# Kernel tuning notes

Measured on AMD Instinct MI355X. Metric: run time of the kernel, lower is better.

Reference implementation:

```python
import jax, jax.numpy as jnp
import numpy as np

N_NODES = 50000
N_EDGES = 1500000
FEAT = 128
CUTOFF = 5.0


def setup_inputs() -> dict:
    key = jax.random.key(0)
    k_x, k_ei, k_el, k_w = jax.random.split(key, 4)
    x = jax.random.normal(k_x, (N_NODES, FEAT), dtype=jnp.float32)
    edge_index = jax.random.randint(k_ei, (2, N_EDGES), 0, N_NODES, dtype=jnp.int64)
    edge_len = jax.random.uniform(k_el, (N_EDGES,), dtype=jnp.float32) * CUTOFF
    # learned params: equivariant mix (dense linear for scalar irreps, no bias),
    # log of distance scale (init sharpness=6.0), and 1->1 filter linear.
    W_mix = jax.random.normal(k_w, (FEAT, FEAT), dtype=jnp.float32) / np.sqrt(FEAT)
    log_scale = jnp.asarray(np.log(6.0), dtype=jnp.float32)
    filter_w = jnp.asarray(0.7, dtype=jnp.float32)
    filter_b = jnp.asarray(0.1, dtype=jnp.float32)
    return {"x": x, "edge_index": edge_index, "edge_len": edge_len,
            "W_mix": W_mix, "log_scale": log_scale,
            "filter_w": filter_w, "filter_b": filter_b}


def reference(x, edge_index, edge_len, W_mix, log_scale, filter_w, filter_b):
    sender = edge_index[0]
    receiver = edge_index[1]
    n_nodes = x.shape[0]

    scale = jnp.exp(log_scale).astype(edge_len.dtype)
    decay = jnp.exp(-jnp.maximum(edge_len / (scale + 1e-6), 0.0) ** 2)  # [E]
    gate = jax.nn.sigmoid(edge_len * filter_w + filter_b)               # [E]
    weights = jnp.nan_to_num(decay * gate, nan=0.0, posinf=0.0, neginf=0.0)

    # gather-scale-scatter: messages [E, F] -> per-node sum
    messages = weights[:, None].astype(x.dtype) * x[sender]
    agg = jax.ops.segment_sum(messages, receiver, num_segments=n_nodes)
    degree = jax.ops.segment_sum(jnp.ones_like(edge_len), receiver,
                                 num_segments=n_nodes)
    agg = agg / jnp.maximum(degree, 1.0)[:, None].astype(x.dtype)

    return x + agg @ W_mix
```

## Files before the change

kernel.cpp:

```cpp
#include <hip/hip_runtime.h>
#include <math.h>

#define FEAT 128
#define BSHIFT 4
#define BNODES 16
#define CAP 1024
#define NBUCK_MAX 4096

__device__ __forceinline__ float edge_weight(float d, float scale, float fw, float fb) {
    float t = fmaxf(d / scale, 0.0f);
    float decay = expf(-t * t);
    float g = 1.0f / (1.0f + expf(-(d * fw + fb)));
    float w = decay * g;
    if (!isfinite(w)) w = 0.0f;
    return w;
}

__device__ __forceinline__ unsigned int bf16_rne(float f) {
    unsigned int b = __float_as_uint(f);
    return (b + 0x7FFFu + ((b >> 16) & 1u)) >> 16;
}

__global__ __launch_bounds__(256) void convert_count_kernel(
    const float4* __restrict__ x4, uint2* __restrict__ xbf, int n4,
    const int* __restrict__ recv, int* __restrict__ sub,
    int E, int nbuck, int epb, int cblocks) {
    __shared__ int cnt[NBUCK_MAX];
    if ((int)blockIdx.x < cblocks) {
        int i = blockIdx.x * 256 + threadIdx.x;
        if (i >= n4) return;
        float4 v = x4[i];
        uint2 o;
        o.x = (bf16_rne(v.y) << 16) | bf16_rne(v.x);
        o.y = (bf16_rne(v.w) << 16) | bf16_rne(v.z);
        xbf[i] = o;
        return;
    }
    int cb = blockIdx.x - cblocks;
    int tid = threadIdx.x;
    for (int i = tid; i < nbuck; i += 256) cnt[i] = 0;
    __syncthreads();
    int base = cb * epb;
    int end = min(base + epb, E);
    for (int e = base + tid; e < end; e += 256)
        atomicAdd(&cnt[recv[e] >> BSHIFT], 1);
    __syncthreads();
    size_t row = (size_t)cb * nbuck;
    for (int i = tid; i < nbuck; i += 256) sub[row + i] = cnt[i];
}

__global__ __launch_bounds__(256) void colscan_kernel(int* __restrict__ sub,
                                                      int* __restrict__ tot,
                                                      int nbuck, int nchunk) {
    __shared__ int vals[256];
    int b = blockIdx.x;
    int tid = threadIdx.x;
    int carry = 0;
    for (int c0 = 0; c0 < nchunk; c0 += 256) {
        int c = c0 + tid;
        int v = (c < nchunk) ? sub[(size_t)c * nbuck + b] : 0;
        vals[tid] = v;
        __syncthreads();
        for (int d = 1; d < 256; d <<= 1) {
            int t = (tid >= d) ? vals[tid - d] : 0;
            __syncthreads();
            vals[tid] += t;
            __syncthreads();
        }
        int excl = vals[tid] - v;
        if (c < nchunk) sub[(size_t)c * nbuck + b] = carry + excl;
        int btot = vals[255];
        __syncthreads();
        carry += btot;
    }
    if (tid == 0) tot[b] = carry;
}

__global__ __launch_bounds__(1024) void scan_kernel(const int* __restrict__ tot,
                                                    int* __restrict__ boff, int M) {
    __shared__ int part[1024];
    int t = threadIdx.x;
    int chunk = (M + 1023) >> 10;
    int lo = t * chunk, hi = min(lo + chunk, M);
    int s = 0;
    for (int i = lo; i < hi; ++i) s += tot[i];
    part[t] = s;
    __syncthreads();
    for (int d = 1; d < 1024; d <<= 1) {
        int v = (t >= d) ? part[t - d] : 0;
        __syncthreads();
        part[t] += v;
        __syncthreads();
    }
    int run = part[t] - s;
    for (int i = lo; i < hi; ++i) {
        boff[i] = run;
        run += tot[i];
    }
    if (hi == M) boff[M] = run;
}

__global__ __launch_bounds__(256) void bucket_scatter_kernel(
    const int* __restrict__ sender, const int* __restrict__ recv,
    const float* __restrict__ edge_len,
    const float* __restrict__ log_scale, const float* __restrict__ filter_w,
    const float* __restrict__ filter_b,
    const int* __restrict__ sub, const int* __restrict__ boff,
    unsigned long long* __restrict__ buf, int E, int nbuck, int epb) {
    __shared__ int cur[NBUCK_MAX];
    int tid = threadIdx.x;
    size_t row = (size_t)blockIdx.x * nbuck;
    for (int i = tid; i < nbuck; i += 256) cur[i] = boff[i] + sub[row + i];
    __syncthreads();
    int base = blockIdx.x * epb;
    int end = min(base + epb, E);
    float scale = expf(log_scale[0]) + 1e-6f;
    float fw = filter_w[0], fb = filter_b[0];
    for (int e = base + tid; e < end; e += 256) {
        int r = recv[e];
        int s = sender[e];
        float w = edge_weight(edge_len[e], scale, fw, fb);
        int pos = atomicAdd(&cur[r >> BSHIFT], 1);
        unsigned long long rec = ((unsigned long long)__float_as_uint(w) << 32)
                               | (unsigned int)(s & 0xFFFF)
                               | ((unsigned int)(r & (BNODES - 1)) << 16);
        buf[pos] = rec;
    }
}

__device__ __forceinline__ void accum8(float acc[8], uint4 u, float w) {
    acc[0] = fmaf(w, __uint_as_float(u.x << 16), acc[0]);
    acc[1] = fmaf(w, __uint_as_float(u.x & 0xFFFF0000u), acc[1]);
    acc[2] = fmaf(w, __uint_as_float(u.y << 16), acc[2]);
    acc[3] = fmaf(w, __uint_as_float(u.y & 0xFFFF0000u), acc[3]);
    acc[4] = fmaf(w, __uint_as_float(u.z << 16), acc[4]);
    acc[5] = fmaf(w, __uint_as_float(u.z & 0xFFFF0000u), acc[5]);
    acc[6] = fmaf(w, __uint_as_float(u.w << 16), acc[6]);
    acc[7] = fmaf(w, __uint_as_float(u.w & 0xFFFF0000u), acc[7]);
}

__global__ __launch_bounds__(256) void bucket_sort_aggregate_kernel(
    const uint4* __restrict__ xbf4, const unsigned long long* __restrict__ buf,
    const int* __restrict__ boff, uint4* __restrict__ agg_bf4,
    int* __restrict__ deg, int N) {
    __shared__ unsigned long long recS[CAP];
    __shared__ int cnt16[BNODES];
    __shared__ int segoff[BNODES + 1];

    int b = blockIdx.x;
    int n0 = b << BSHIFT;
    int nEnd = min(n0 + BNODES, N);
    int lo = boff[b], hi = boff[b + 1];
    int tid = threadIdx.x;
    int lane = tid & 15;
    int grp = tid >> 4;

    float acc[8] = {0.f,0.f,0.f,0.f,0.f,0.f,0.f,0.f};
    int dcnt = 0;

    for (int pos = lo; pos < hi; pos += CAP) {
        int cnt = min(CAP, hi - pos);
        if (tid < BNODES) cnt16[tid] = 0;
        __syncthreads();

        unsigned long long rec[CAP / 256];
        int rnk[CAP / 256];
        int locl[CAP / 256];
#pragma unroll
        for (int k = 0; k < CAP / 256; ++k) {
            int i = k * 256 + tid;
            if (i < cnt) {
                unsigned long long r = buf[pos + i];
                int l = ((unsigned int)r >> 16) & (BNODES - 1);
                rec[k] = r;
                locl[k] = l;
                rnk[k] = atomicAdd(&cnt16[l], 1);
            }
        }
        __syncthreads();
        if (tid == 0) {
            int run = 0;
#pragma unroll
            for (int l = 0; l < BNODES; ++l) { segoff[l] = run; run += cnt16[l]; }
            segoff[BNODES] = run;
        }
        __syncthreads();
#pragma unroll
        for (int k = 0; k < CAP / 256; ++k) {
            int i = k * 256 + tid;
            if (i < cnt) recS[segoff[locl[k]] + rnk[k]] = rec[k];
        }
        __syncthreads();

        {
            int s0 = segoff[grp], s1 = segoff[grp + 1];
            dcnt += s1 - s0;
            int i = s0;
            for (; i + 4 <= s1; i += 4) {
                unsigned long long r0 = recS[i];
                unsigned long long r1 = recS[i + 1];
                unsigned long long r2 = recS[i + 2];
                unsigned long long r3 = recS[i + 3];
                float w0 = __uint_as_float((unsigned int)(r0 >> 32));
                float w1 = __uint_as_float((unsigned int)(r1 >> 32));
                float w2 = __uint_as_float((unsigned int)(r2 >> 32));
                float w3 = __uint_as_float((unsigned int)(r3 >> 32));
                int s0i = (unsigned int)r0 & 0xFFFF;
                int s1i = (unsigned int)r1 & 0xFFFF;
                int s2i = (unsigned int)r2 & 0xFFFF;
                int s3i = (unsigned int)r3 & 0xFFFF;
                uint4 u0 = xbf4[(size_t)s0i * 16 + lane];
                uint4 u1 = xbf4[(size_t)s1i * 16 + lane];
                uint4 u2 = xbf4[(size_t)s2i * 16 + lane];
                uint4 u3 = xbf4[(size_t)s3i * 16 + lane];
                accum8(acc, u0, w0);
                accum8(acc, u1, w1);
                accum8(acc, u2, w2);
                accum8(acc, u3, w3);
            }
            for (; i < s1; ++i) {
                unsigned long long ra = recS[i];
                float wa = __uint_as_float((unsigned int)(ra >> 32));
                int sa = (unsigned int)ra & 0xFFFF;
                uint4 ua = xbf4[(size_t)sa * 16 + lane];
                accum8(acc, ua, wa);
            }
        }
        __syncthreads();
    }

    {
        int n = n0 + grp;
        if (n < nEnd) {
            uint4 o;
            o.x = (bf16_rne(acc[1]) << 16) | bf16_rne(acc[0]);
            o.y = (bf16_rne(acc[3]) << 16) | bf16_rne(acc[2]);
            o.z = (bf16_rne(acc[5]) << 16) | bf16_rne(acc[4]);
            o.w = (bf16_rne(acc[7]) << 16) | bf16_rne(acc[6]);
            agg_bf4[(size_t)n * 16 + lane] = o;
            if (lane == 0) deg[n] = dcnt;
        }
    }
}

__global__ __launch_bounds__(256) void finalize_kernel(
    const float* __restrict__ x, const uint4* __restrict__ agg_bf4,
    const int* __restrict__ deg, const float* __restrict__ Wm,
    float* __restrict__ out, int N) {
    __shared__ float aggS[64 * 128];
    __shared__ float Ws[128 * 64];
    const int n0 = blockIdx.x * 64;

    for (int i = threadIdx.x; i < 64 * 16; i += 256) {
        int r = i >> 4;
        int q = i & 15;
        int n = n0 + r;
        uint4 u = make_uint4(0u, 0u, 0u, 0u);
        if (n < N) u = agg_bf4[(size_t)n * 16 + q];
        float4 f0, f1;
        f0.x = __uint_as_float(u.x << 16);
        f0.y = __uint_as_float(u.x & 0xFFFF0000u);
        f0.z = __uint_as_float(u.y << 16);
        f0.w = __uint_as_float(u.y & 0xFFFF0000u);
        f1.x = __uint_as_float(u.z << 16);
        f1.y = __uint_as_float(u.z & 0xFFFF0000u);
        f1.z = __uint_as_float(u.w << 16);
        f1.w = __uint_as_float(u.w & 0xFFFF0000u);
        int m = (r >> 2) & 7;
        ((float4*)aggS)[r * 32 + ((2 * q) ^ m)] = f0;
        ((float4*)aggS)[r * 32 + ((2 * q + 1) ^ m)] = f1;
    }

    const int tc = threadIdx.x & 15;
    const int tr = threadIdx.x >> 4;

    float invd[4];
#pragma unroll
    for (int i = 0; i < 4; ++i) {
        int n = n0 + 4 * tr + i;
        float degf = 1.0f;
        if (n < N) degf = fmaxf((float)deg[n], 1.0f);
        invd[i] = 1.0f / degf;
    }

    for (int h = 0; h < 2; ++h) {
        for (int i = threadIdx.x; i < 128 * 16; i += 256) {
            int k = i >> 4;
            int j4 = i & 15;
            ((float4*)Ws)[k * 16 + j4] = ((const float4*)Wm)[k * 32 + h * 16 + j4];
        }
        __syncthreads();

        float acc[4][4];
#pragma unroll
        for (int i = 0; i < 4; ++i)
#pragma unroll
            for (int c = 0; c < 4; ++c) acc[i][c] = 0.f;

#pragma unroll 4
        for (int k0 = 0; k0 < 128; k0 += 4) {
            float4 ar4[4];
            const int chunk = (k0 >> 2) ^ (tr & 7);
#pragma unroll
            for (int i = 0; i < 4; ++i) {
                int r = 4 * tr + i;
                ar4[i] = ((const float4*)aggS)[r * 32 + chunk];
            }
            float4 wv4[4];
#pragma unroll
            for (int kk = 0; kk < 4; ++kk)
                wv4[kk] = *(const float4*)&Ws[(k0 + kk) * 64 + tc * 4];

            float wvv[4][4];
#pragma unroll
            for (int kk = 0; kk < 4; ++kk) {
                wvv[kk][0] = wv4[kk].x; wvv[kk][1] = wv4[kk].y;
                wvv[kk][2] = wv4[kk].z; wvv[kk][3] = wv4[kk].w;
            }
#pragma unroll
            for (int i = 0; i < 4; ++i) {
                float av[4] = {ar4[i].x, ar4[i].y, ar4[i].z, ar4[i].w};
#pragma unroll
                for (int kk = 0; kk < 4; ++kk)
#pragma unroll
                    for (int c = 0; c < 4; ++c)
                        acc[i][c] = fmaf(av[kk], wvv[kk][c], acc[i][c]);
            }
        }

#pragma unroll
        for (int i = 0; i < 4; ++i) {
            int n = n0 + 4 * tr + i;
            if (n < N) {
                size_t base = (size_t)n * FEAT + h * 64 + tc * 4;
                float4 xv = *(const float4*)&x[base];
                float4 o;
                o.x = xv.x + invd[i] * acc[i][0];
                o.y = xv.y + invd[i] * acc[i][1];
                o.z = xv.z + invd[i] * acc[i][2];
                o.w = xv.w + invd[i] * acc[i][3];
                *(float4*)&out[base] = o;
            }
        }
        __syncthreads();
    }
}

__global__ __launch_bounds__(256) void scatter_fallback(
    const float4* __restrict__ x4, const int* __restrict__ sender,
    const int* __restrict__ receiver, const float* __restrict__ edge_len,
    const float* __restrict__ log_scale, const float* __restrict__ filter_w,
    const float* __restrict__ filter_b, float* __restrict__ agg,
    float* __restrict__ deg, int E) {
    int gid = blockIdx.x * 256 + threadIdx.x;
    int e = gid >> 5;
    if (e >= E) return;
    int lane = gid & 31;
    int s = sender[e];
    int r = receiver[e];
    float scale = expf(log_scale[0]) + 1e-6f;
    float w = edge_weight(edge_len[e], scale, filter_w[0], filter_b[0]);
    float4 xv = x4[s * (FEAT / 4) + lane];
    float* dst = agg + (size_t)r * FEAT + lane * 4;
    unsafeAtomicAdd(dst + 0, w * xv.x);
    unsafeAtomicAdd(dst + 1, w * xv.y);
    unsafeAtomicAdd(dst + 2, w * xv.z);
    unsafeAtomicAdd(dst + 3, w * xv.w);
    if (lane == 0) unsafeAtomicAdd(&deg[r], 1.0f);
}

__global__ __launch_bounds__(256) void finalize_fallback(
    const float* __restrict__ x, const float* __restrict__ agg,
    const float* __restrict__ deg, const float* __restrict__ Wm,
    float* __restrict__ out, int N) {
    __shared__ float Wsf[FEAT * FEAT];
    for (int i = threadIdx.x * 4; i < FEAT * FEAT; i += 256 * 4)
        *(float4*)&Wsf[i] = *(const float4*)&Wm[i];
    __syncthreads();
    int half = threadIdx.x >> 7;
    int j = threadIdx.x & (FEAT - 1);
    for (int n0 = blockIdx.x * 2; n0 < N; n0 += gridDim.x * 2) {
        int n = n0 + half;
        if (n < N) {
            const float* arow = agg + (size_t)n * FEAT;
            float acc = 0.0f;
#pragma unroll 16
            for (int k = 0; k < FEAT; ++k) acc = fmaf(arow[k], Wsf[k * FEAT + j], acc);
            float invd = 1.0f / fmaxf(deg[n], 1.0f);
            size_t idx = (size_t)n * FEAT + j;
            out[idx] = x[idx] + invd * acc;
        }
    }
}

extern "C" void kernel_launch(void* const* d_in, const int* in_sizes, int n_in,
                              void* d_out, int out_size, void* d_ws, size_t ws_size,
                              hipStream_t stream) {
    const float* x         = (const float*)d_in[0];
    const int*   ei        = (const int*)d_in[1];
    const float* edge_len  = (const float*)d_in[2];
    const float* W_mix     = (const float*)d_in[3];
    const float* log_scale = (const float*)d_in[4];
    const float* filter_w  = (const float*)d_in[5];
    const float* filter_b  = (const float*)d_in[6];
    float* out = (float*)d_out;

    const int N = in_sizes[0] / FEAT;
    const int E = in_sizes[1] / 2;
    const int* sender   = ei;
    const int* receiver = ei + E;
    const int nbuck = (N + BNODES - 1) >> BSHIFT;

    size_t xbf_bytes  = (size_t)N * FEAT * 2;
    size_t aggb_bytes = (size_t)N * FEAT * 2;
    size_t buf_bytes  = (size_t)E * 8;
    size_t tot_bytes  = (((size_t)nbuck * 4) + 63) & ~(size_t)63;
    size_t boff_bytes = (((size_t)(nbuck + 1) * 4) + 63) & ~(size_t)63;
    size_t deg_bytes  = (((size_t)N * 4) + 63) & ~(size_t)63;
    size_t fixed = xbf_bytes + aggb_bytes + buf_bytes + tot_bytes + boff_bytes +
                   deg_bytes;

    int epb = 0, nchunk = 0;
    size_t sub_bytes = 0;
    const int epb_opts[3] = {4096, 8192, 16384};
    for (int oi = 0; oi < 3; ++oi) {
        int cand = epb_opts[oi];
        int nc = (E + cand - 1) / cand;
        size_t sb = (((size_t)nc * nbuck * 4) + 63) & ~(size_t)63;
        if (fixed + sb <= ws_size) { epb = cand; nchunk = nc; sub_bytes = sb; break; }
    }

    if (epb != 0 && N <= 65536) {
        char* p = (char*)d_ws;
        uint2* xbf    = (uint2*)p;                        p += xbf_bytes;
        uint4* agg_bf = (uint4*)p;                        p += aggb_bytes;
        unsigned long long* buf = (unsigned long long*)p; p += buf_bytes;
        int* sub  = (int*)p;                              p += sub_bytes;
        int* tot  = (int*)p;                              p += tot_bytes;
        int* boff = (int*)p;                              p += boff_bytes;
        int* deg  = (int*)p;

        int cblocks = (N * (FEAT / 4) + 255) / 256;
        convert_count_kernel<<<cblocks + nchunk, 256, 0, stream>>>(
            (const float4*)x, xbf, N * (FEAT / 4),
            receiver, sub, E, nbuck, epb, cblocks);
        colscan_kernel<<<nbuck, 256, 0, stream>>>(sub, tot, nbuck, nchunk);
        scan_kernel<<<1, 1024, 0, stream>>>(tot, boff, nbuck);
        bucket_scatter_kernel<<<nchunk, 256, 0, stream>>>(
            sender, receiver, edge_len, log_scale, filter_w, filter_b,
            sub, boff, buf, E, nbuck, epb);
        bucket_sort_aggregate_kernel<<<nbuck, 256, 0, stream>>>(
            (const uint4*)xbf, buf, boff, agg_bf, deg, N);
        int fblocks = (N + 63) / 64;
        finalize_kernel<<<fblocks, 256, 0, stream>>>(x, (const uint4*)agg_bf, deg,
                                                     W_mix, out, N);
    } else {
        float* agg = (float*)d_ws;
        float* degf = agg + (size_t)N * FEAT;
        hipMemsetAsync(agg, 0, ((size_t)N * FEAT + N) * sizeof(float), stream);
        int sblocks = (E * 32 + 255) / 256;
        scatter_fallback<<<sblocks, 256, 0, stream>>>(
            (const float4*)x, sender, receiver, edge_len,
            log_scale, filter_w, filter_b, agg, degf, E);
        finalize_fallback<<<512, 256, 0, stream>>>(x, agg, degf, W_mix, out, N);
    }
}
```

Measured before the change: 238.6 us.

## Replace bucketed two-level sort with per-node CSR via global atomics

Switches from the 16-node bucket sort (per-chunk shared histograms, column scan, and an in-block local sort) to a direct per-receiver CSR: global atomic degree counts, a single scan over nodes, atomic per-node scatter, and an aggregate kernel that reads each node's contiguous edge list with 8-deep prefetch. This removes the colscan kernel, the large sub-count matrix and the shared-memory re-sort in aggregation. The cost is contended global atomics over 50k counters in both the count and scatter passes, a single-block scan over 50k entries, and an extra memset.

```diff
diff --git a/kernel.cpp b/kernel.cpp
--- a/kernel.cpp
+++ b/kernel.cpp
@@ -4,8 +4,6 @@
 #define FEAT 128
 #define BSHIFT 4
 #define BNODES 16
-#define CAP 1024
-#define NBUCK_MAX 4096
 
 __device__ __forceinline__ float edge_weight(float d, float scale, float fw, float fb) {
     float t = fmaxf(d / scale, 0.0f);
@@ -23,9 +21,7 @@
 
 __global__ __launch_bounds__(256) void convert_count_kernel(
     const float4* __restrict__ x4, uint2* __restrict__ xbf, int n4,
-    const int* __restrict__ recv, int* __restrict__ sub,
-    int E, int nbuck, int epb, int cblocks) {
-    __shared__ int cnt[NBUCK_MAX];
+    const int* __restrict__ recv, int* __restrict__ deg, int E, int cblocks) {
     if ((int)blockIdx.x < cblocks) {
         int i = blockIdx.x * 256 + threadIdx.x;
         if (i >= n4) return;
@@ -36,54 +32,21 @@
         xbf[i] = o;
         return;
     }
-    int cb = blockIdx.x - cblocks;
-    int tid = threadIdx.x;
-    for (int i = tid; i < nbuck; i += 256) cnt[i] = 0;
-    __syncthreads();
-    int base = cb * epb;
-    int end = min(base + epb, E);
-    for (int e = base + tid; e < end; e += 256)
-        atomicAdd(&cnt[recv[e] >> BSHIFT], 1);
-    __syncthreads();
-    size_t row = (size_t)cb * nbuck;
-    for (int i = tid; i < nbuck; i += 256) sub[row + i] = cnt[i];
-}
-
-__global__ __launch_bounds__(256) void colscan_kernel(int* __restrict__ sub,
-                                                      int* __restrict__ tot,
-                                                      int nbuck, int nchunk) {
-    __shared__ int vals[256];
-    int b = blockIdx.x;
-    int tid = threadIdx.x;
-    int carry = 0;
-    for (int c0 = 0; c0 < nchunk; c0 += 256) {
-        int c = c0 + tid;
-        int v = (c < nchunk) ? sub[(size_t)c * nbuck + b] : 0;
-        vals[tid] = v;
-        __syncthreads();
-        for (int d = 1; d < 256; d <<= 1) {
-            int t = (tid >= d) ? vals[tid - d] : 0;
-            __syncthreads();
-            vals[tid] += t;
-            __syncthreads();
-        }
-        int excl = vals[tid] - v;
-        if (c < nchunk) sub[(size_t)c * nbuck + b] = carry + excl;
-        int btot = vals[255];
-        __syncthreads();
-        carry += btot;
-    }
-    if (tid == 0) tot[b] = carry;
-}
-
-__global__ __launch_bounds__(1024) void scan_kernel(const int* __restrict__ tot,
-                                                    int* __restrict__ boff, int M) {
+    int nb = gridDim.x - cblocks;
+    int gid = ((int)blockIdx.x - cblocks) * 256 + threadIdx.x;
+    for (int e = gid; e < E; e += nb * 256)
+        atomicAdd(&deg[recv[e]], 1);
+}
+
+__global__ __launch_bounds__(1024) void scan_kernel(const int* __restrict__ deg,
+                                                    int* __restrict__ noff,
+                                                    int* __restrict__ ncur, int M) {
     __shared__ int part[1024];
     int t = threadIdx.x;
     int chunk = (M + 1023) >> 10;
-    int lo = t * chunk, hi = min(lo + chunk, M);
+    int lo = min(t * chunk, M), hi = min(lo + chunk, M);
     int s = 0;
-    for (int i = lo; i < hi; ++i) s += tot[i];
+    for (int i = lo; i < hi; ++i) s += deg[i];
     part[t] = s;
     __syncthreads();
     for (int d = 1; d < 1024; d <<= 1) {
@@ -94,37 +57,29 @@
     }
     int run = part[t] - s;
     for (int i = lo; i < hi; ++i) {
-        boff[i] = run;
-        run += tot[i];
-    }
-    if (hi == M) boff[M] = run;
-}
-
-__global__ __launch_bounds__(256) void bucket_scatter_kernel(
+        noff[i] = run;
+        ncur[i] = run;
+        run += deg[i];
+    }
+    if (hi == M) noff[M] = run;
+}
+
+__global__ __launch_bounds__(256) void scatter_kernel(
     const int* __restrict__ sender, const int* __restrict__ recv,
     const float* __restrict__ edge_len,
     const float* __restrict__ log_scale, const float* __restrict__ filter_w,
     const float* __restrict__ filter_b,
-    const int* __restrict__ sub, const int* __restrict__ boff,
-    unsigned long long* __restrict__ buf, int E, int nbuck, int epb) {
-    __shared__ int cur[NBUCK_MAX];
-    int tid = threadIdx.x;
-    size_t row = (size_t)blockIdx.x * nbuck;
-    for (int i = tid; i < nbuck; i += 256) cur[i] = boff[i] + sub[row + i];
-    __syncthreads();
-    int base = blockIdx.x * epb;
-    int end = min(base + epb, E);
+    int* __restrict__ ncur, unsigned long long* __restrict__ buf, int E) {
     float scale = expf(log_scale[0]) + 1e-6f;
     float fw = filter_w[0], fb = filter_b[0];
-    for (int e = base + tid; e < end; e += 256) {
+    int stride = gridDim.x * 256;
+    for (int e = blockIdx.x * 256 + threadIdx.x; e < E; e += stride) {
         int r = recv[e];
         int s = sender[e];
         float w = edge_weight(edge_len[e], scale, fw, fb);
-        int pos = atomicAdd(&cur[r >> BSHIFT], 1);
-        unsigned long long rec = ((unsigned long long)__float_as_uint(w) << 32)
-                               | (unsigned int)(s & 0xFFFF)
-                               | ((unsigned int)(r & (BNODES - 1)) << 16);
-        buf[pos] = rec;
+        int pos = atomicAdd(&ncur[r], 1);
+        buf[pos] = ((unsigned long long)__float_as_uint(w) << 32)
+                 | (unsigned int)s;
     }
 }
 
@@ -139,108 +94,52 @@
     acc[7] = fmaf(w, __uint_as_float(u.w & 0xFFFF0000u), acc[7]);
 }
 
-__global__ __launch_bounds__(256) void bucket_sort_aggregate_kernel(
+__global__ __launch_bounds__(256) void aggregate_kernel(
     const uint4* __restrict__ xbf4, const unsigned long long* __restrict__ buf,
-    const int* __restrict__ boff, uint4* __restrict__ agg_bf4,
-    int* __restrict__ deg, int N) {
-    __shared__ unsigned long long recS[CAP];
-    __shared__ int cnt16[BNODES];
-    __shared__ int segoff[BNODES + 1];
-
-    int b = blockIdx.x;
-    int n0 = b << BSHIFT;
-    int nEnd = min(n0 + BNODES, N);
-    int lo = boff[b], hi = boff[b + 1];
-    int tid = threadIdx.x;
-    int lane = tid & 15;
-    int grp = tid >> 4;
-
-    float acc[8] = {0.f,0.f,0.f,0.f,0.f,0.f,0.f,0.f};
-    int dcnt = 0;
-
-    for (int pos = lo; pos < hi; pos += CAP) {
-        int cnt = min(CAP, hi - pos);
-        if (tid < BNODES) cnt16[tid] = 0;
-        __syncthreads();
-
-        unsigned long long rec[CAP / 256];
-        int rnk[CAP / 256];
-        int locl[CAP / 256];
-#pragma unroll
-        for (int k = 0; k < CAP / 256; ++k) {
-            int i = k * 256 + tid;
-            if (i < cnt) {
-                unsigned long long r = buf[pos + i];
-                int l = ((unsigned int)r >> 16) & (BNODES - 1);
-                rec[k] = r;
-                locl[k] = l;
-                rnk[k] = atomicAdd(&cnt16[l], 1);
-            }
-        }
-        __syncthreads();
-        if (tid == 0) {
-            int run = 0;
-#pragma unroll
-            for (int l = 0; l < BNODES; ++l) { segoff[l] = run; run += cnt16[l]; }
-            segoff[BNODES] = run;
-        }
-        __syncthreads();
-#pragma unroll
-        for (int k = 0; k < CAP / 256; ++k) {
-            int i = k * 256 + tid;
-            if (i < cnt) recS[segoff[locl[k]] + rnk[k]] = rec[k];
-        }
-        __syncthreads();
-
-        {
-            int s0 = segoff[grp], s1 = segoff[grp + 1];
-            dcnt += s1 - s0;
-            int i = s0;
-            for (; i + 4 <= s1; i += 4) {
-                unsigned long long r0 = recS[i];
-                unsigned long long r1 = recS[i + 1];
-                unsigned long long r2 = recS[i + 2];
-                unsigned long long r3 = recS[i + 3];
-                float w0 = __uint_as_float((unsigned int)(r0 >> 32));
-                float w1 = __uint_as_float((unsigned int)(r1 >> 32));
-                float w2 = __uint_as_float((unsigned int)(r2 >> 32));
-                float w3 = __uint_as_float((unsigned int)(r3 >> 32));
-                int s0i = (unsigned int)r0 & 0xFFFF;
-                int s1i = (unsigned int)r1 & 0xFFFF;
-                int s2i = (unsigned int)r2 & 0xFFFF;
-                int s3i = (unsigned int)r3 & 0xFFFF;
-                uint4 u0 = xbf4[(size_t)s0i * 16 + lane];
-                uint4 u1 = xbf4[(size_t)s1i * 16 + lane];
-                uint4 u2 = xbf4[(size_t)s2i * 16 + lane];
-                uint4 u3 = xbf4[(size_t)s3i * 16 + lane];
-                accum8(acc, u0, w0);
-                accum8(acc, u1, w1);
-                accum8(acc, u2, w2);
-                accum8(acc, u3, w3);
-            }
-            for (; i < s1; ++i) {
-                unsigned long long ra = recS[i];
-                float wa = __uint_as_float((unsigned int)(ra >> 32));
-                int sa = (unsigned int)ra & 0xFFFF;
-                uint4 ua = xbf4[(size_t)sa * 16 + lane];
-                accum8(acc, ua, wa);
-            }
-        }
-        __syncthreads();
-    }
-
-    {
-        int n = n0 + grp;
-        if (n < nEnd) {
-            uint4 o;
-            o.x = (bf16_rne(acc[1]) << 16) | bf16_rne(acc[0]);
-            o.y = (bf16_rne(acc[3]) << 16) | bf16_rne(acc[2]);
-            o.z = (bf16_rne(acc[5]) << 16) | bf16_rne(acc[4]);
-            o.w = (bf16_rne(acc[7]) << 16) | bf16_rne(acc[6]);
-            agg_bf4[(size_t)n * 16 + lane] = o;
-            if (lane == 0) deg[n] = dcnt;
-        }
-    }
+    const int* __restrict__ noff, uint4* __restrict__ agg_bf4, int N) {
+    int n = ((int)blockIdx.x << BSHIFT) + (threadIdx.x >> 4);
+    int lane = threadIdx.x & 15;
+    if (n >= N) return;
+    int i = noff[n];
+    int e1 = noff[n + 1];
+
+    float acc[8] = {0.f, 0.f, 0.f, 0.f, 0.f, 0.f, 0.f, 0.f};
+
+    unsigned long long r[8];
+#pragma unroll
+    for (int k = 0; k < 8; ++k) {
+        unsigned long long v = buf[i + k];
+        r[k] = (i + k < e1) ? v : 0ULL;
+    }
+    while (i < e1) {
+        float w[8];
+        int sx[8];
+#pragma unroll
+        for (int k = 0; k < 8; ++k) {
+            w[k] = __uint_as_float((unsigned int)(r[k] >> 32));
+            sx[k] = (int)((unsigned int)r[k] & 0xFFFFu);
+        }
+        uint4 u[8];
+#pragma unroll
+        for (int k = 0; k < 8; ++k)
+            u[k] = xbf4[(size_t)sx[k] * 16 + lane];
+        int inext = i + 8;
+#pragma unroll
+        for (int k = 0; k < 8; ++k) {
+            unsigned long long v = buf[inext + k];
+            r[k] = (inext + k < e1) ? v : 0ULL;
+        }
+#pragma unroll
+        for (int k = 0; k < 8; ++k) accum8(acc, u[k], w[k]);
+        i = inext;
+    }
+
+    uint4 o;
+    o.x = (bf16_rne(acc[1]) << 16) | bf16_rne(acc[0]);
+    o.y = (bf16_rne(acc[3]) << 16) | bf16_rne(acc[2]);
+    o.z = (bf16_rne(acc[5]) << 16) | bf16_rne(acc[4]);
+    o.w = (bf16_rne(acc[7]) << 16) | bf16_rne(acc[6]);
+    agg_bf4[(size_t)n * 16 + lane] = o;
 }
 
 __global__ __launch_bounds__(256) void finalize_kernel(
@@ -413,44 +312,35 @@
 
     size_t xbf_bytes  = (size_t)N * FEAT * 2;
     size_t aggb_bytes = (size_t)N * FEAT * 2;
-    size_t buf_bytes  = (size_t)E * 8;
-    size_t tot_bytes  = (((size_t)nbuck * 4) + 63) & ~(size_t)63;
-    size_t boff_bytes = (((size_t)(nbuck + 1) * 4) + 63) & ~(size_t)63;
-    size_t deg_bytes  = (((size_t)N * 4) + 63) & ~(size_t)63;
-    size_t fixed = xbf_bytes + aggb_bytes + buf_bytes + tot_bytes + boff_bytes +
-                   deg_bytes;
-
-    int epb = 0, nchunk = 0;
-    size_t sub_bytes = 0;
-    const int epb_opts[3] = {4096, 8192, 16384};
-    for (int oi = 0; oi < 3; ++oi) {
-        int cand = epb_opts[oi];
-        int nc = (E + cand - 1) / cand;
-        size_t sb = (((size_t)nc * nbuck * 4) + 63) & ~(size_t)63;
-        if (fixed + sb <= ws_size) { epb = cand; nchunk = nc; sub_bytes = sb; break; }
-    }
-
-    if (epb != 0 && N <= 65536) {
+    size_t buf_bytes  = ((size_t)E + 16) * 8;
+    size_t deg_bytes  = (((size_t)(N + 1) * 4) + 63) & ~(size_t)63;
+    size_t noff_bytes = (((size_t)(N + 1) * 4) + 63) & ~(size_t)63;
+    size_t ncur_bytes = (((size_t)(N + 1) * 4) + 63) & ~(size_t)63;
+    size_t fixed = xbf_bytes + aggb_bytes + buf_bytes + deg_bytes + noff_bytes +
+                   ncur_bytes;
+
+    if (fixed <= ws_size && N <= 65536) {
         char* p = (char*)d_ws;
         uint2* xbf    = (uint2*)p;                        p += xbf_bytes;
         uint4* agg_bf = (uint4*)p;                        p += aggb_bytes;
         unsigned long long* buf = (unsigned long long*)p; p += buf_bytes;
-        int* sub  = (int*)p;                              p += sub_bytes;
-        int* tot  = (int*)p;                              p += tot_bytes;
-        int* boff = (int*)p;                              p += boff_bytes;
-        int* deg  = (int*)p;
-
-        int cblocks = (N * (FEAT / 4) + 255) / 256;
-        convert_count_kernel<<<cblocks + nchunk, 256, 0, stream>>>(
-            (const float4*)x, xbf, N * (FEAT / 4),
-            receiver, sub, E, nbuck, epb, cblocks);
-        colscan_kernel<<<nbuck, 256, 0, stream>>>(sub, tot, nbuck, nchunk);
-        scan_kernel<<<1, 1024, 0, stream>>>(tot, boff, nbuck);
-        bucket_scatter_kernel<<<nchunk, 256, 0, stream>>>(
+        int* deg  = (int*)p;                              p += deg_bytes;
+        int* noff = (int*)p;                              p += noff_bytes;
+        int* ncur = (int*)p;
+
+        hipMemsetAsync(deg, 0, (size_t)(N + 1) * sizeof(int), stream);
+
+        int n4 = N * (FEAT / 4);
+        int cblocks = (n4 + 255) / 256;
+        int countb = 1024;
+        convert_count_kernel<<<cblocks + countb, 256, 0, stream>>>(
+            (const float4*)x, xbf, n4, receiver, deg, E, cblocks);
+        scan_kernel<<<1, 1024, 0, stream>>>(deg, noff, ncur, N);
+        scatter_kernel<<<2048, 256, 0, stream>>>(
             sender, receiver, edge_len, log_scale, filter_w, filter_b,
-            sub, boff, buf, E, nbuck, epb);
-        bucket_sort_aggregate_kernel<<<nbuck, 256, 0, stream>>>(
-            (const uint4*)xbf, buf, boff, agg_bf, deg, N);
+            ncur, buf, E);
+        aggregate_kernel<<<nbuck, 256, 0, stream>>>(
+            (const uint4*)xbf, buf, noff, agg_bf, N);
         int fblocks = (N + 63) / 64;
         finalize_kernel<<<fblocks, 256, 0, stream>>>(x, (const uint4*)agg_bf, deg,
                                                      W_mix, out, N);
```

Result: slower. 475.5 us (+99.3%).

## Use 64-node coarse buckets with four sub-blocks each and a per-thread column scan

Applied to the files above, without the earlier changes.

Coarse buckets now cover 64 nodes, so the count and scatter kernels handle about 782 buckets instead of 3125. The sub-count matrix shrinks, and so do the shared-memory histogram init and write-back. The aggregate kernel launches four blocks per coarse bucket. Each block reads the whole bucket's record list but keeps only its 16-node quarter. The column scan becomes one thread per bucket walking the chunks serially, replacing the block-wide shared-memory scan. The cost is that every edge record is now read four times in the aggregate phase, and the serial column scan may have poor memory coalescing per chunk.

```diff
diff --git a/kernel.cpp b/kernel.cpp
--- a/kernel.cpp
+++ b/kernel.cpp
@@ -2,10 +2,12 @@
 #include <math.h>
 
 #define FEAT 128
-#define BSHIFT 4
-#define BNODES 16
+#define BSHIFT 6
+#define BNODES 64
+#define FB 16
 #define CAP 1024
-#define NBUCK_MAX 4096
+#define NBUCK_MAX 1024
+#define EPB 8192
 
 __device__ __forceinline__ float edge_weight(float d, float scale, float fw, float fb) {
     float t = fmaxf(d / scale, 0.0f);
@@ -24,7 +26,7 @@
 __global__ __launch_bounds__(256) void convert_count_kernel(
     const float4* __restrict__ x4, uint2* __restrict__ xbf, int n4,
     const int* __restrict__ recv, int* __restrict__ sub,
-    int E, int nbuck, int epb, int cblocks) {
+    int E, int nbuck, int cblocks) {
     __shared__ int cnt[NBUCK_MAX];
     if ((int)blockIdx.x < cblocks) {
         int i = blockIdx.x * 256 + threadIdx.x;
@@ -40,8 +42,8 @@
     int tid = threadIdx.x;
     for (int i = tid; i < nbuck; i += 256) cnt[i] = 0;
     __syncthreads();
-    int base = cb * epb;
-    int end = min(base + epb, E);
+    int base = cb * EPB;
+    int end = min(base + EPB, E);
     for (int e = base + tid; e < end; e += 256)
         atomicAdd(&cnt[recv[e] >> BSHIFT], 1);
     __syncthreads();
@@ -52,28 +54,26 @@
 __global__ __launch_bounds__(256) void colscan_kernel(int* __restrict__ sub,
                                                       int* __restrict__ tot,
                                                       int nbuck, int nchunk) {
-    __shared__ int vals[256];
-    int b = blockIdx.x;
-    int tid = threadIdx.x;
+    int b = blockIdx.x * 256 + threadIdx.x;
+    if (b >= nbuck) return;
     int carry = 0;
-    for (int c0 = 0; c0 < nchunk; c0 += 256) {
-        int c = c0 + tid;
-        int v = (c < nchunk) ? sub[(size_t)c * nbuck + b] : 0;
-        vals[tid] = v;
-        __syncthreads();
-        for (int d = 1; d < 256; d <<= 1) {
-            int t = (tid >= d) ? vals[tid - d] : 0;
-            __syncthreads();
-            vals[tid] += t;
-            __syncthreads();
-        }
-        int excl = vals[tid] - v;
-        if (c < nchunk) sub[(size_t)c * nbuck + b] = carry + excl;
-        int btot = vals[255];
-        __syncthreads();
-        carry += btot;
-    }
-    if (tid == 0) tot[b] = carry;
+    int c = 0;
+    for (; c + 8 <= nchunk; c += 8) {
+        int v[8];
+#pragma unroll
+        for (int k = 0; k < 8; ++k) v[k] = sub[(size_t)(c + k) * nbuck + b];
+#pragma unroll
+        for (int k = 0; k < 8; ++k) {
+            sub[(size_t)(c + k) * nbuck + b] = carry;
+            carry += v[k];
+        }
+    }
+    for (; c < nchunk; ++c) {
+        int v = sub[(size_t)c * nbuck + b];
+        sub[(size_t)c * nbuck + b] = carry;
+        carry += v;
+    }
+    tot[b] = carry;
 }
 
 __global__ __launch_bounds__(1024) void scan_kernel(const int* __restrict__ tot,
@@ -81,7 +81,7 @@
     __shared__ int part[1024];
     int t = threadIdx.x;
     int chunk = (M + 1023) >> 10;
-    int lo = t * chunk, hi = min(lo + chunk, M);
+    int lo = min(t * chunk, M), hi = min(lo + chunk, M);
     int s = 0;
     for (int i = lo; i < hi; ++i) s += tot[i];
     part[t] = s;
@@ -106,14 +106,14 @@
     const float* __restrict__ log_scale, const float* __restrict__ filter_w,
     const float* __restrict__ filter_b,
     const int* __restrict__ sub, const int* __restrict__ boff,
-    unsigned long long* __restrict__ buf, int E, int nbuck, int epb) {
+    unsigned long long* __restrict__ buf, int E, int nbuck) {
     __shared__ int cur[NBUCK_MAX];
     int tid = threadIdx.x;
     size_t row = (size_t)blockIdx.x * nbuck;
     for (int i = tid; i < nbuck; i += 256) cur[i] = boff[i] + sub[row + i];
     __syncthreads();
-    int base = blockIdx.x * epb;
-    int end = min(base + epb, E);
+    int base = blockIdx.x * EPB;
+    int end = min(base + EPB, E);
     float scale = expf(log_scale[0]) + 1e-6f;
     float fw = filter_w[0], fb = filter_b[0];
     for (int e = base + tid; e < end; e += 256) {
@@ -144,13 +144,14 @@
     const int* __restrict__ boff, uint4* __restrict__ agg_bf4,
     int* __restrict__ deg, int N) {
     __shared__ unsigned long long recS[CAP];
-    __shared__ int cnt16[BNODES];
-    __shared__ int segoff[BNODES + 1];
-
-    int b = blockIdx.x;
-    int n0 = b << BSHIFT;
-    int nEnd = min(n0 + BNODES, N);
-    int lo = boff[b], hi = boff[b + 1];
+    __shared__ int cnt16[FB];
+    __shared__ int segoff[FB + 1];
+
+    int cb = blockIdx.x >> 2;
+    int q  = blockIdx.x & 3;
+    int n0 = (cb << BSHIFT) + (q << 4);
+    int nEnd = min(n0 + FB, N);
+    int lo = boff[cb], hi = boff[cb + 1];
     int tid = threadIdx.x;
     int lane = tid & 15;
     int grp = tid >> 4;
@@ -160,36 +161,37 @@
 
     for (int pos = lo; pos < hi; pos += CAP) {
         int cnt = min(CAP, hi - pos);
-        if (tid < BNODES) cnt16[tid] = 0;
+        if (tid < FB) cnt16[tid] = 0;
         __syncthreads();
 
         unsigned long long rec[CAP / 256];
-        int rnk[CAP / 256];
-        int locl[CAP / 256];
+        int lr[CAP / 256];
 #pragma unroll
         for (int k = 0; k < CAP / 256; ++k) {
             int i = k * 256 + tid;
+            lr[k] = -1;
             if (i < cnt) {
                 unsigned long long r = buf[pos + i];
-                int l = ((unsigned int)r >> 16) & (BNODES - 1);
-                rec[k] = r;
-                locl[k] = l;
-                rnk[k] = atomicAdd(&cnt16[l], 1);
+                int l6 = ((unsigned int)r >> 16) & 63;
+                if ((l6 >> 4) == q) {
+                    int l = l6 & 15;
+                    int rk = atomicAdd(&cnt16[l], 1);
+                    lr[k] = (rk << 4) | l;
+                    rec[k] = r;
+                }
             }
         }
         __syncthreads();
         if (tid == 0) {
             int run = 0;
 #pragma unroll
-            for (int l = 0; l < BNODES; ++l) { segoff[l] = run; run += cnt16[l]; }
-            segoff[BNODES] = run;
-        }
-        __syncthreads();
-#pragma unroll
-        for (int k = 0; k < CAP / 256; ++k) {
-            int i = k * 256 + tid;
-            if (i < cnt) recS[segoff[locl[k]] + rnk[k]] = rec[k];
-        }
+            for (int l = 0; l < FB; ++l) { segoff[l] = run; run += cnt16[l]; }
+            segoff[FB] = run;
+        }
+        __syncthreads();
+#pragma unroll
+        for (int k = 0; k < CAP / 256; ++k)
+            if (lr[k] >= 0) recS[segoff[lr[k] & 15] + (lr[k] >> 4)] = rec[k];
         __syncthreads();
 
         {
@@ -410,27 +412,19 @@
     const int* sender   = ei;
     const int* receiver = ei + E;
     const int nbuck = (N + BNODES - 1) >> BSHIFT;
+    const int nchunk = (E + EPB - 1) / EPB;
 
     size_t xbf_bytes  = (size_t)N * FEAT * 2;
     size_t aggb_bytes = (size_t)N * FEAT * 2;
-    size_t buf_bytes  = (size_t)E * 8;
+    size_t buf_bytes  = ((size_t)E + 16) * 8;
+    size_t sub_bytes  = (((size_t)nchunk * nbuck * 4) + 63) & ~(size_t)63;
     size_t tot_bytes  = (((size_t)nbuck * 4) + 63) & ~(size_t)63;
     size_t boff_bytes = (((size_t)(nbuck + 1) * 4) + 63) & ~(size_t)63;
     size_t deg_bytes  = (((size_t)N * 4) + 63) & ~(size_t)63;
-    size_t fixed = xbf_bytes + aggb_bytes + buf_bytes + tot_bytes + boff_bytes +
-                   deg_bytes;
-
-    int epb = 0, nchunk = 0;
-    size_t sub_bytes = 0;
-    const int epb_opts[3] = {4096, 8192, 16384};
-    for (int oi = 0; oi < 3; ++oi) {
-        int cand = epb_opts[oi];
-        int nc = (E + cand - 1) / cand;
-        size_t sb = (((size_t)nc * nbuck * 4) + 63) & ~(size_t)63;
-        if (fixed + sb <= ws_size) { epb = cand; nchunk = nc; sub_bytes = sb; break; }
-    }
-
-    if (epb != 0 && N <= 65536) {
+    size_t fixed = xbf_bytes + aggb_bytes + buf_bytes + sub_bytes + tot_bytes +
+                   boff_bytes + deg_bytes;
+
+    if (fixed <= ws_size && N <= 65536) {
         char* p = (char*)d_ws;
         uint2* xbf    = (uint2*)p;                        p += xbf_bytes;
         uint4* agg_bf = (uint4*)p;                        p += aggb_bytes;
@@ -440,16 +434,17 @@
         int* boff = (int*)p;                              p += boff_bytes;
         int* deg  = (int*)p;
 
-        int cblocks = (N * (FEAT / 4) + 255) / 256;
+        int n4 = N * (FEAT / 4);
+        int cblocks = (n4 + 255) / 256;
         convert_count_kernel<<<cblocks + nchunk, 256, 0, stream>>>(
-            (const float4*)x, xbf, N * (FEAT / 4),
-            receiver, sub, E, nbuck, epb, cblocks);
-        colscan_kernel<<<nbuck, 256, 0, stream>>>(sub, tot, nbuck, nchunk);
+            (const float4*)x, xbf, n4, receiver, sub, E, nbuck, cblocks);
+        colscan_kernel<<<(nbuck + 255) / 256, 256, 0, stream>>>(sub, tot, nbuck,
+                                                                nchunk);
         scan_kernel<<<1, 1024, 0, stream>>>(tot, boff, nbuck);
         bucket_scatter_kernel<<<nchunk, 256, 0, stream>>>(
             sender, receiver, edge_len, log_scale, filter_w, filter_b,
-            sub, boff, buf, E, nbuck, epb);
-        bucket_sort_aggregate_kernel<<<nbuck, 256, 0, stream>>>(
+            sub, boff, buf, E, nbuck);
+        bucket_sort_aggregate_kernel<<<nbuck * 4, 256, 0, stream>>>(
             (const uint4*)xbf, buf, boff, agg_bf, deg, N);
         int fblocks = (N + 63) / 64;
         finalize_kernel<<<fblocks, 256, 0, stream>>>(x, (const uint4*)agg_bf, deg,
```

Result: no change. 238.4 us (-0.0%).
